# Kernel optimization log

Hardware: AMD Instinct MI355X
Metric: run time of the kernel (lower is better)

Reference implementation:

```python
import jax, jax.numpy as jnp
import numpy as np

B, TQ, TK, D, DV = 16, 2048, 2048, 128, 128
MASK_VAL = -1000000.0

def setup_inputs() -> dict:
    key = jax.random.key(0)
    kq, kk, kv, kl = jax.random.split(key, 4)
    q = jax.random.normal(kq, (B, TQ, D), dtype=jnp.float32)
    k = jax.random.normal(kk, (B, TK, D), dtype=jnp.float32)
    v = jax.random.normal(kv, (B, TK, DV), dtype=jnp.float32)
    valid_lens = jax.random.randint(kl, (B,), 1, TK, dtype=jnp.int64)
    return {"q": q, "k": k, "v": v, "valid_lens": valid_lens}

def reference(q, k, v, valid_lens):
    d = q.shape[-1]
    # scores: [B, Tq, Tk]
    scores = jnp.einsum('bqd,bkd->bqk', q, k) / jnp.sqrt(jnp.asarray(d, q.dtype))
    # mask key positions >= valid_len (same per-batch length for every query row)
    mask = jnp.arange(scores.shape[-1])[None, None, :] < valid_lens[:, None, None]
    scores = jnp.where(mask, scores, jnp.asarray(MASK_VAL, scores.dtype))
    attn = jax.nn.softmax(scores, axis=-1)
    # dropout p=0.0 (eval mode) -> identity
    return jnp.einsum('bqk,bkv->bqv', attn, v)
```

## Files before the change

### kernel.cpp

```cpp
#include <hip/hip_runtime.h>
#include <math.h>

#define NB 16
#define TQ 2048
#define TK 2048
#define DD 128
#define DVV 128

constexpr int QTILE = 128;
constexpr int KTILE = 32;
#define PSTR 40

typedef __attribute__((ext_vector_type(8))) _Float16 half8;
typedef __attribute__((ext_vector_type(4))) _Float16 half4;
typedef __attribute__((ext_vector_type(4))) float f32x4;

__device__ inline float fast_exp2(float x) {
#if __has_builtin(__builtin_amdgcn_exp2f)
    return __builtin_amdgcn_exp2f(x);
#else
    return exp2f(x);
#endif
}
__device__ inline void setprio1() { __builtin_amdgcn_s_setprio(1); }
__device__ inline void setprio0() { __builtin_amdgcn_s_setprio(0); }

__device__ inline void glds16(const _Float16* g, _Float16* l) {
    __builtin_amdgcn_global_load_lds(
        (const __attribute__((address_space(1))) void*)g,
        (__attribute__((address_space(3))) void*)l, 16, 0, 0);
}

__global__ __launch_bounds__(256)
void repack(const float* __restrict__ kg, const float* __restrict__ vg,
            const int* __restrict__ vlg,
            _Float16* __restrict__ Kpk, _Float16* __restrict__ Vpk)
{
    const int bt = blockIdx.x;
    const int b = bt >> 6, t = bt & 63;
    if (t * KTILE >= vlg[b]) return;
    const int tid = threadIdx.x;

    __shared__ float Vlds[32][129];

    const float* kin = kg + ((size_t)b * TK + t * KTILE) * DD;
    _Float16* kout = Kpk + ((size_t)bt << 12);
#pragma unroll
    for (int pp = 0; pp < 2; ++pp) {
        int s = tid + pp * 256;
        int ct = s >> 8, c = (s >> 6) & 3, ln = s & 63;
        int kr = ct * 16 + (ln & 15), kc = c * 32 + ((ln >> 4) & 3) * 8;
        const float* ip = kin + kr * DD + kc;
        float4 f0 = *(const float4*)ip;
        float4 f1 = *(const float4*)(ip + 4);
        half8 h;
        h[0] = (_Float16)f0.x; h[1] = (_Float16)f0.y;
        h[2] = (_Float16)f0.z; h[3] = (_Float16)f0.w;
        h[4] = (_Float16)f1.x; h[5] = (_Float16)f1.y;
        h[6] = (_Float16)f1.z; h[7] = (_Float16)f1.w;
        *(half8*)(kout + (size_t)s * 8) = h;
    }

    const float* vin = vg + ((size_t)b * TK + t * KTILE) * DVV;
#pragma unroll
    for (int pp = 0; pp < 4; ++pp) {
        int idx = tid + pp * 256;
        int r = idx >> 5, c4 = (idx & 31) * 4;
        float4 f = *(const float4*)(vin + r * DVV + c4);
        Vlds[r][c4 + 0] = f.x; Vlds[r][c4 + 1] = f.y;
        Vlds[r][c4 + 2] = f.z; Vlds[r][c4 + 3] = f.w;
    }
    __syncthreads();
    _Float16* vout = Vpk + ((size_t)bt << 12);
#pragma unroll
    for (int pp = 0; pp < 2; ++pp) {
        int s = tid + pp * 256;
        int n = s >> 6, ln = s & 63;
        int dv = n * 16 + (ln & 15), k0 = ((ln >> 4) & 3) * 8;
        half8 h;
#pragma unroll
        for (int j = 0; j < 8; ++j)
            h[j] = (_Float16)Vlds[k0 + j][dv];
        *(half8*)(vout + (size_t)s * 8) = h;
    }
}

__global__ __launch_bounds__(512, 6)
void attn_fwd(const float* __restrict__ qg,
              const _Float16* __restrict__ Kpk, const _Float16* __restrict__ Vpk,
              const int* __restrict__ vlg,
              float* __restrict__ outg, _Float16* __restrict__ wso,
              float* __restrict__ wsml, int ns)
{
    __shared__ _Float16 Kb[2][4096];
    __shared__ _Float16 Vb[2][4096];
    __shared__ _Float16 Plds[8][16][PSTR];

    const int tid  = threadIdx.x;
    const int wid  = tid >> 6;
    const int lane = tid & 63;
    const int l15  = lane & 15;
    const int lhi  = lane >> 4;

    const int bid   = blockIdx.x;
    const int b     = bid & (NB - 1);
    const int qbase = (bid >> 4) * QTILE;
    const int sp    = blockIdx.y;

    const int VL  = vlg[b];
    const int nkt = (VL + KTILE - 1) / KTILE;
    const int tps = (nkt + ns - 1) / ns;
    const int t0  = sp * tps;
    const int t1  = min(nkt, t0 + tps);
    if (t0 >= t1) return;

    const _Float16* ktb = Kpk + ((size_t)(b * 64) << 12);
    const _Float16* vtb = Vpk + ((size_t)(b * 64) << 12);

    half8 qf[4];
    {
        const float scale = 0.08838834764831845f * 1.4426950408889634f;
        const int qrow = qbase + wid * 16 + l15;
        const float* qp = qg + (size_t)(b * TQ + qrow) * DD + lhi * 8;
#pragma unroll
        for (int c = 0; c < 4; ++c) {
            float4 f0 = *(const float4*)(qp + c * 32);
            float4 f1 = *(const float4*)(qp + c * 32 + 4);
            half8 t;
            t[0] = (_Float16)(f0.x * scale); t[1] = (_Float16)(f0.y * scale);
            t[2] = (_Float16)(f0.z * scale); t[3] = (_Float16)(f0.w * scale);
            t[4] = (_Float16)(f1.x * scale); t[5] = (_Float16)(f1.y * scale);
            t[6] = (_Float16)(f1.z * scale); t[7] = (_Float16)(f1.w * scale);
            qf[c] = t;
        }
    }

    const int qtr = wid & 3;
    auto STAGE = [&](int buf, int t) {
        const _Float16* src = ((wid < 4) ? ktb : vtb)
                              + ((size_t)t << 12) + qtr * 1024 + lane * 8;
        _Float16* dst = (wid < 4) ? &Kb[buf][qtr * 1024] : &Vb[buf][qtr * 1024];
        glds16(src, dst);
        glds16(src + 512, dst + 512);
    };

    float m_i = -INFINITY, l_i = 0.f;
    f32x4 o[8];
#pragma unroll
    for (int n = 0; n < 8; ++n) { f32x4 z = {0.f, 0.f, 0.f, 0.f}; o[n] = z; }

    STAGE(0, t0);
    int cur = 0;
    for (int t = t0; t < t1; ++t) {
        const int kb = t * KTILE;
        const bool pre = (t + 1 < t1);
        if (pre) STAGE(cur ^ 1, t + 1);

        if (pre) asm volatile("s_waitcnt vmcnt(2)\ns_barrier" ::: "memory");
        else     asm volatile("s_waitcnt vmcnt(0)\ns_barrier" ::: "memory");

        const half8* kp = (const half8*)&Kb[cur][0];
        const half8* vp = (const half8*)&Vb[cur][0];

        f32x4 sc[2];
        setprio1();
#pragma unroll
        for (int ct = 0; ct < 2; ++ct) {
            f32x4 z = {0.f, 0.f, 0.f, 0.f};
            sc[ct] = z;
#pragma unroll
            for (int c = 0; c < 4; ++c) {
                half8 kf = kp[ct * 256 + c * 64 + lane];
                sc[ct] = __builtin_amdgcn_mfma_f32_16x16x32_f16(kf, qf[c], sc[ct], 0, 0, 0);
            }
        }
        setprio0();

        if (kb + KTILE > VL) {
#pragma unroll
            for (int ct = 0; ct < 2; ++ct) {
                const int kg = kb + ct * 16 + lhi * 4;
#pragma unroll
                for (int r = 0; r < 4; ++r)
                    if (kg + r >= VL) sc[ct][r] = -1e30f;
            }
        }

        float mx = sc[0][0];
#pragma unroll
        for (int ct = 0; ct < 2; ++ct)
#pragma unroll
            for (int r = 0; r < 4; ++r) mx = fmaxf(mx, sc[ct][r]);
        mx = fmaxf(mx, __shfl_xor(mx, 16));
        mx = fmaxf(mx, __shfl_xor(mx, 32));

        const bool skip = __all(mx <= m_i + 8.0f);
        const float mnew = skip ? m_i : fmaxf(m_i, mx);

        float p[8];
        float sum = 0.f;
#pragma unroll
        for (int ct = 0; ct < 2; ++ct)
#pragma unroll
            for (int r = 0; r < 4; ++r) {
                float e = fast_exp2(sc[ct][r] - mnew);
                p[ct * 4 + r] = e;
                sum += e;
            }
        sum += __shfl_xor(sum, 16);
        sum += __shfl_xor(sum, 32);

#pragma unroll
        for (int ct = 0; ct < 2; ++ct) {
            half4 ph;
            ph[0] = (_Float16)p[ct * 4 + 0]; ph[1] = (_Float16)p[ct * 4 + 1];
            ph[2] = (_Float16)p[ct * 4 + 2]; ph[3] = (_Float16)p[ct * 4 + 3];
            *(half4*)&Plds[wid][l15][ct * 16 + lhi * 4] = ph;
        }

        if (skip) {
            l_i += sum;
        } else {
            const float corr = fast_exp2(m_i - mnew);
            l_i = l_i * corr + sum;
            m_i = mnew;
            float cr[4];
#pragma unroll
            for (int r = 0; r < 4; ++r)
                cr[r] = __shfl(corr, (lane & 48) | (lhi * 4 + r));
#pragma unroll
            for (int n = 0; n < 8; ++n)
#pragma unroll
                for (int r = 0; r < 4; ++r) o[n][r] *= cr[r];
        }

        half8 pa = *(const half8*)&Plds[wid][l15][lhi * 8];
        setprio1();
#pragma unroll
        for (int n = 0; n < 8; ++n) {
            half8 vb = vp[n * 64 + lane];
            o[n] = __builtin_amdgcn_mfma_f32_16x16x32_f16(pa, vb, o[n], 0, 0, 0);
        }
        setprio0();

        asm volatile("s_waitcnt lgkmcnt(0)\ns_barrier" ::: "memory");
        cur ^= 1;
    }

    if (ns == 1) {
        float li4[4];
#pragma unroll
        for (int r = 0; r < 4; ++r) {
            float lr = __shfl(l_i, (lane & 48) | (lhi * 4 + r));
            li4[r] = 1.0f / lr;
        }
#pragma unroll
        for (int r = 0; r < 4; ++r) {
            const int qrow = qbase + wid * 16 + lhi * 4 + r;
            float* op = outg + (size_t)(b * TQ + qrow) * DVV + l15;
#pragma unroll
            for (int n = 0; n < 8; ++n)
                op[n * 16] = o[n][r] * li4[r];
        }
    } else {
        if (lhi == 0) {
            float2 ml = make_float2(m_i, l_i);
            *(float2*)&wsml[((size_t)(sp * NB + b) * TQ + qbase + wid * 16 + l15) * 2] = ml;
        }
        _Float16* po = wso + ((size_t)(sp * NB + b) * TQ + qbase + wid * 16) * DVV;
#pragma unroll
        for (int r = 0; r < 4; ++r)
#pragma unroll
            for (int n = 0; n < 8; ++n)
                po[(lhi * 4 + r) * DVV + n * 16 + l15] = (_Float16)o[n][r];
    }
}

__global__ __launch_bounds__(256)
void attn_combine(const _Float16* __restrict__ wso, const float* __restrict__ wsml,
                  const int* __restrict__ vlg, float* __restrict__ outg, int ns)
{
    const int idx = blockIdx.x * 256 + threadIdx.x;
    const int d8 = idx & 15;
    const int q  = (idx >> 4) & (TQ - 1);
    const int b  = idx >> 15;

    const int VL  = vlg[b];
    const int nkt = (VL + KTILE - 1) / KTILE;
    const int tps = (nkt + ns - 1) / ns;
    const int nv  = (nkt + tps - 1) / tps;

    float M = -1e30f, den = 0.f;
    float acc[8] = {0.f, 0.f, 0.f, 0.f, 0.f, 0.f, 0.f, 0.f};
    for (int s = 0; s < nv; ++s) {
        const size_t row = (size_t)(s * NB + b) * TQ + q;
        float2 ml = *(const float2*)&wsml[row * 2];
        float Mn = fmaxf(M, ml.x);
        float c  = fast_exp2(M - Mn);
        float w  = fast_exp2(ml.x - Mn);
        half8 ov = *(const half8*)&wso[row * DVV + d8 * 8];
#pragma unroll
        for (int j = 0; j < 8; ++j)
            acc[j] = acc[j] * c + (float)ov[j] * w;
        den = den * c + w * ml.y;
        M = Mn;
    }
    const float inv = 1.0f / den;
    float* op = outg + ((size_t)b * TQ + q) * DVV + d8 * 8;
    f32x4 r0 = {acc[0] * inv, acc[1] * inv, acc[2] * inv, acc[3] * inv};
    f32x4 r1 = {acc[4] * inv, acc[5] * inv, acc[6] * inv, acc[7] * inv};
    *(f32x4*)op = r0;
    *(f32x4*)(op + 4) = r1;
}

extern "C" void kernel_launch(void* const* d_in, const int* in_sizes, int n_in,
                              void* d_out, int out_size, void* d_ws, size_t ws_size,
                              hipStream_t stream) {
    const float* q  = (const float*)d_in[0];
    const float* k  = (const float*)d_in[1];
    const float* v  = (const float*)d_in[2];
    const int*   vl = (const int*)d_in[3];
    float* out = (float*)d_out;

    const size_t pk_elems = (size_t)NB * 64 * 4096;
    const size_t pk_bytes = 2 * pk_elems * sizeof(_Float16);
    const size_t o_elems  = (size_t)NB * TQ * DVV;
    const size_t ml_elems = (size_t)NB * TQ * 2;
    const size_t per_split = o_elems * sizeof(_Float16) + ml_elems * sizeof(float);

    int ns = 1;
    if (ws_size >= pk_bytes + 4 * per_split) ns = 4;
    else if (ws_size >= pk_bytes + 2 * per_split) ns = 2;

    _Float16* Kpk = (_Float16*)d_ws;
    _Float16* Vpk = Kpk + pk_elems;
    _Float16* wso  = Vpk + pk_elems;
    float*    wsml = (float*)(wso + (size_t)ns * o_elems);

    hipLaunchKernelGGL(repack, dim3(NB * 64), dim3(256), 0, stream,
                       k, v, vl, Kpk, Vpk);

    dim3 grid(NB * (TQ / QTILE), ns);
    hipLaunchKernelGGL(attn_fwd, grid, dim3(512), 0, stream,
                       q, Kpk, Vpk, vl, out, wso, wsml, ns);

    if (ns > 1) {
        dim3 cgrid((NB * TQ * 16) / 256);
        hipLaunchKernelGGL(attn_combine, cgrid, dim3(256), 0, stream,
                           wso, wsml, vl, out, ns);
    }
}
```

Before: 71.71 us.

## Switch attention to 32x32x16 MFMA with in-register P exchange and fixed-size KV splits

Moves QK^T and PV from 16x16x32 to 32x32x16 MFMA tiles, with each wave handling 32 query rows and the block shrunk to 4 waves. K and V are repacked to match. The P matrix is now converted to fp16 and exchanged between half-waves with cross-lane shuffles instead of a round trip through LDS, and the output is transposed through LDS so stores coalesce. KV splitting now uses a fixed tiles-per-split size (up to 8 splits) so short sequences launch fewer active blocks, at the cost of more accumulator registers per wave and lower occupancy.

Result: slower. 75.01 us (+4.6%).

```diff
diff --git a/kernel.cpp b/kernel.cpp
--- a/kernel.cpp
+++ b/kernel.cpp
@@ -7,23 +7,23 @@
 #define DD 128
 #define DVV 128
 
+constexpr int KTILE = 32;
 constexpr int QTILE = 128;
-constexpr int KTILE = 32;
-#define PSTR 40
 
 typedef __attribute__((ext_vector_type(8))) _Float16 half8;
-typedef __attribute__((ext_vector_type(4))) _Float16 half4;
+typedef __attribute__((ext_vector_type(16))) float f32x16;
 typedef __attribute__((ext_vector_type(4))) float f32x4;
 
-__device__ inline float fast_exp2(float x) {
-#if __has_builtin(__builtin_amdgcn_exp2f)
-    return __builtin_amdgcn_exp2f(x);
-#else
-    return exp2f(x);
-#endif
-}
+__device__ inline float fast_exp2(float x) { return __builtin_amdgcn_exp2f(x); }
 __device__ inline void setprio1() { __builtin_amdgcn_s_setprio(1); }
 __device__ inline void setprio0() { __builtin_amdgcn_s_setprio(0); }
+
+__device__ inline unsigned pk2(float a, float b) {
+    auto h = __builtin_amdgcn_cvt_pkrtz(a, b);
+    unsigned u;
+    __builtin_memcpy(&u, &h, 4);
+    return u;
+}
 
 __device__ inline void glds16(const _Float16* g, _Float16* l) {
     __builtin_amdgcn_global_load_lds(
@@ -48,17 +48,17 @@
 #pragma unroll
     for (int pp = 0; pp < 2; ++pp) {
         int s = tid + pp * 256;
-        int ct = s >> 8, c = (s >> 6) & 3, ln = s & 63;
-        int kr = ct * 16 + (ln & 15), kc = c * 32 + ((ln >> 4) & 3) * 8;
-        const float* ip = kin + kr * DD + kc;
+        int c = s >> 6, l = s & 63;
+        int row = l & 31, d0 = c * 16 + (l >> 5) * 8;
+        const float* ip = kin + row * DD + d0;
         float4 f0 = *(const float4*)ip;
         float4 f1 = *(const float4*)(ip + 4);
-        half8 h;
-        h[0] = (_Float16)f0.x; h[1] = (_Float16)f0.y;
-        h[2] = (_Float16)f0.z; h[3] = (_Float16)f0.w;
-        h[4] = (_Float16)f1.x; h[5] = (_Float16)f1.y;
-        h[6] = (_Float16)f1.z; h[7] = (_Float16)f1.w;
-        *(half8*)(kout + (size_t)s * 8) = h;
+        half8 hh;
+        hh[0] = (_Float16)f0.x; hh[1] = (_Float16)f0.y;
+        hh[2] = (_Float16)f0.z; hh[3] = (_Float16)f0.w;
+        hh[4] = (_Float16)f1.x; hh[5] = (_Float16)f1.y;
+        hh[6] = (_Float16)f1.z; hh[7] = (_Float16)f1.w;
+        *(half8*)(kout + (size_t)s * 8) = hh;
     }
 
     const float* vin = vg + ((size_t)b * TK + t * KTILE) * DVV;
@@ -75,79 +75,79 @@
 #pragma unroll
     for (int pp = 0; pp < 2; ++pp) {
         int s = tid + pp * 256;
-        int n = s >> 6, ln = s & 63;
-        int dv = n * 16 + (ln & 15), k0 = ((ln >> 4) & 3) * 8;
-        half8 h;
+        int sv = s >> 6, l = s & 63;
+        int dv = (sv >> 1) * 32 + (l & 31);
+        int k0 = (sv & 1) * 16 + (l >> 5) * 8;
+        half8 hh;
 #pragma unroll
         for (int j = 0; j < 8; ++j)
-            h[j] = (_Float16)Vlds[k0 + j][dv];
-        *(half8*)(vout + (size_t)s * 8) = h;
-    }
-}
-
-__global__ __launch_bounds__(512, 6)
+            hh[j] = (_Float16)Vlds[k0 + j][dv];
+        *(half8*)(vout + (size_t)s * 8) = hh;
+    }
+}
+
+__global__ __launch_bounds__(256, 3)
 void attn_fwd(const float* __restrict__ qg,
               const _Float16* __restrict__ Kpk, const _Float16* __restrict__ Vpk,
               const int* __restrict__ vlg,
               float* __restrict__ outg, _Float16* __restrict__ wso,
-              float* __restrict__ wsml, int ns)
+              float* __restrict__ wsml, int nsplit, int tpb)
 {
-    __shared__ _Float16 Kb[2][4096];
-    __shared__ _Float16 Vb[2][4096];
-    __shared__ _Float16 Plds[8][16][PSTR];
+    __shared__ __align__(16) _Float16 smem[16384];
 
     const int tid  = threadIdx.x;
     const int wid  = tid >> 6;
     const int lane = tid & 63;
-    const int l15  = lane & 15;
-    const int lhi  = lane >> 4;
-
-    const int bid   = blockIdx.x;
-    const int b     = bid & (NB - 1);
-    const int qbase = (bid >> 4) * QTILE;
+    const int l31  = lane & 31;
+    const int hi   = lane >> 5;
+
+    const int b     = blockIdx.x & (NB - 1);
+    const int qbase = (blockIdx.x >> 4) * QTILE;
     const int sp    = blockIdx.y;
 
     const int VL  = vlg[b];
     const int nkt = (VL + KTILE - 1) / KTILE;
-    const int tps = (nkt + ns - 1) / ns;
-    const int t0  = sp * tps;
-    const int t1  = min(nkt, t0 + tps);
+    const int t0  = sp * tpb;
+    const int t1  = min(nkt, t0 + tpb);
     if (t0 >= t1) return;
 
     const _Float16* ktb = Kpk + ((size_t)(b * 64) << 12);
     const _Float16* vtb = Vpk + ((size_t)(b * 64) << 12);
 
-    half8 qf[4];
+    half8 qf[8];
     {
         const float scale = 0.08838834764831845f * 1.4426950408889634f;
-        const int qrow = qbase + wid * 16 + l15;
-        const float* qp = qg + (size_t)(b * TQ + qrow) * DD + lhi * 8;
-#pragma unroll
-        for (int c = 0; c < 4; ++c) {
-            float4 f0 = *(const float4*)(qp + c * 32);
-            float4 f1 = *(const float4*)(qp + c * 32 + 4);
-            half8 t;
-            t[0] = (_Float16)(f0.x * scale); t[1] = (_Float16)(f0.y * scale);
-            t[2] = (_Float16)(f0.z * scale); t[3] = (_Float16)(f0.w * scale);
-            t[4] = (_Float16)(f1.x * scale); t[5] = (_Float16)(f1.y * scale);
-            t[6] = (_Float16)(f1.z * scale); t[7] = (_Float16)(f1.w * scale);
-            qf[c] = t;
-        }
-    }
-
-    const int qtr = wid & 3;
+        const float* qp = qg + (size_t)(b * TQ + qbase + wid * 32 + l31) * DD;
+#pragma unroll
+        for (int c = 0; c < 8; ++c) {
+            int d0 = c * 16 + hi * 8;
+            float4 f0 = *(const float4*)(qp + d0);
+            float4 f1 = *(const float4*)(qp + d0 + 4);
+            half8 tq;
+            tq[0] = (_Float16)(f0.x * scale); tq[1] = (_Float16)(f0.y * scale);
+            tq[2] = (_Float16)(f0.z * scale); tq[3] = (_Float16)(f0.w * scale);
+            tq[4] = (_Float16)(f1.x * scale); tq[5] = (_Float16)(f1.y * scale);
+            tq[6] = (_Float16)(f1.z * scale); tq[7] = (_Float16)(f1.w * scale);
+            qf[c] = tq;
+        }
+    }
+
     auto STAGE = [&](int buf, int t) {
-        const _Float16* src = ((wid < 4) ? ktb : vtb)
-                              + ((size_t)t << 12) + qtr * 1024 + lane * 8;
-        _Float16* dst = (wid < 4) ? &Kb[buf][qtr * 1024] : &Vb[buf][qtr * 1024];
-        glds16(src, dst);
-        glds16(src + 512, dst + 512);
+        const bool isK = wid < 2;
+        const int hf = wid & 1;
+        const _Float16* src = (isK ? ktb : vtb) + ((size_t)t << 12) + hf * 2048 + lane * 8;
+        _Float16* dst = smem + (isK ? 0 : 8192) + buf * 4096 + hf * 2048;
+#pragma unroll
+        for (int u = 0; u < 4; ++u)
+            glds16(src + u * 512, dst + u * 512);
     };
 
     float m_i = -INFINITY, l_i = 0.f;
-    f32x4 o[8];
-#pragma unroll
-    for (int n = 0; n < 8; ++n) { f32x4 z = {0.f, 0.f, 0.f, 0.f}; o[n] = z; }
+    f32x16 o[4];
+#pragma unroll
+    for (int n = 0; n < 4; ++n)
+#pragma unroll
+        for (int r = 0; r < 16; ++r) o[n][r] = 0.f;
 
     STAGE(0, t0);
     int cur = 0;
@@ -156,67 +156,61 @@
         const bool pre = (t + 1 < t1);
         if (pre) STAGE(cur ^ 1, t + 1);
 
-        if (pre) asm volatile("s_waitcnt vmcnt(2)\ns_barrier" ::: "memory");
+        if (pre) asm volatile("s_waitcnt vmcnt(4)\ns_barrier" ::: "memory");
         else     asm volatile("s_waitcnt vmcnt(0)\ns_barrier" ::: "memory");
 
-        const half8* kp = (const half8*)&Kb[cur][0];
-        const half8* vp = (const half8*)&Vb[cur][0];
-
-        f32x4 sc[2];
+        const _Float16* kbuf = smem + cur * 4096;
+        const _Float16* vbuf = smem + 8192 + cur * 4096;
+
+        f32x16 sc;
+#pragma unroll
+        for (int r = 0; r < 16; ++r) sc[r] = 0.f;
         setprio1();
 #pragma unroll
-        for (int ct = 0; ct < 2; ++ct) {
-            f32x4 z = {0.f, 0.f, 0.f, 0.f};
-            sc[ct] = z;
-#pragma unroll
-            for (int c = 0; c < 4; ++c) {
-                half8 kf = kp[ct * 256 + c * 64 + lane];
-                sc[ct] = __builtin_amdgcn_mfma_f32_16x16x32_f16(kf, qf[c], sc[ct], 0, 0, 0);
+        for (int c = 0; c < 8; ++c) {
+            half8 kf = *(const half8*)(kbuf + c * 512 + lane * 8);
+            sc = __builtin_amdgcn_mfma_f32_32x32x16_f16(kf, qf[c], sc, 0, 0, 0);
+        }
+        setprio0();
+
+        if (kb + KTILE > VL) {
+#pragma unroll
+            for (int r = 0; r < 16; ++r) {
+                int rowk = kb + (r & 3) + 8 * (r >> 2) + 4 * hi;
+                if (rowk >= VL) sc[r] = -1e30f;
             }
         }
-        setprio0();
-
-        if (kb + KTILE > VL) {
-#pragma unroll
-            for (int ct = 0; ct < 2; ++ct) {
-                const int kg = kb + ct * 16 + lhi * 4;
-#pragma unroll
-                for (int r = 0; r < 4; ++r)
-                    if (kg + r >= VL) sc[ct][r] = -1e30f;
-            }
-        }
-
-        float mx = sc[0][0];
-#pragma unroll
-        for (int ct = 0; ct < 2; ++ct)
-#pragma unroll
-            for (int r = 0; r < 4; ++r) mx = fmaxf(mx, sc[ct][r]);
-        mx = fmaxf(mx, __shfl_xor(mx, 16));
+
+        float mx = sc[0];
+#pragma unroll
+        for (int r = 1; r < 16; ++r) mx = fmaxf(mx, sc[r]);
         mx = fmaxf(mx, __shfl_xor(mx, 32));
 
         const bool skip = __all(mx <= m_i + 8.0f);
         const float mnew = skip ? m_i : fmaxf(m_i, mx);
 
-        float p[8];
+        float p[16];
         float sum = 0.f;
 #pragma unroll
-        for (int ct = 0; ct < 2; ++ct)
-#pragma unroll
-            for (int r = 0; r < 4; ++r) {
-                float e = fast_exp2(sc[ct][r] - mnew);
-                p[ct * 4 + r] = e;
-                sum += e;
-            }
-        sum += __shfl_xor(sum, 16);
+        for (int r = 0; r < 16; ++r) {
+            p[r] = fast_exp2(sc[r] - mnew);
+            sum += p[r];
+        }
         sum += __shfl_xor(sum, 32);
 
-#pragma unroll
-        for (int ct = 0; ct < 2; ++ct) {
-            half4 ph;
-            ph[0] = (_Float16)p[ct * 4 + 0]; ph[1] = (_Float16)p[ct * 4 + 1];
-            ph[2] = (_Float16)p[ct * 4 + 2]; ph[3] = (_Float16)p[ct * 4 + 3];
-            *(half4*)&Plds[wid][l15][ct * 16 + lhi * 4] = ph;
-        }
+        unsigned a0 = pk2(p[0],  p[1]),  a1 = pk2(p[2],  p[3]);
+        unsigned a2 = pk2(p[4],  p[5]),  a3 = pk2(p[6],  p[7]);
+        unsigned b0 = pk2(p[8],  p[9]),  b1 = pk2(p[10], p[11]);
+        unsigned b2 = pk2(p[12], p[13]), b3 = pk2(p[14], p[15]);
+        unsigned pa0 = __shfl_xor(a0, 32), pa1 = __shfl_xor(a1, 32);
+        unsigned pa2 = __shfl_xor(a2, 32), pa3 = __shfl_xor(a3, 32);
+        unsigned pb0 = __shfl_xor(b0, 32), pb1 = __shfl_xor(b1, 32);
+        unsigned pb2 = __shfl_xor(b2, 32), pb3 = __shfl_xor(b3, 32);
+        union PF { unsigned u[4]; half8 v; } pf0, pf1;
+        pf0.u[0] = hi ? pa2 : a0;  pf0.u[1] = hi ? pa3 : a1;
+        pf0.u[2] = hi ? a2  : pa0; pf0.u[3] = hi ? a3  : pa1;
+        pf1.u[0] = hi ? pb2 : b0;  pf1.u[1] = hi ? pb3 : b1;
+        pf1.u[2] = hi ? b2  : pb0; pf1.u[3] = hi ? b3  : pb1;
 
         if (skip) {
             l_i += sum;
@@ -224,22 +218,19 @@
             const float corr = fast_exp2(m_i - mnew);
             l_i = l_i * corr + sum;
             m_i = mnew;
-            float cr[4];
-#pragma unroll
-            for (int r = 0; r < 4; ++r)
-                cr[r] = __shfl(corr, (lane & 48) | (lhi * 4 + r));
-#pragma unroll
-            for (int n = 0; n < 8; ++n)
-#pragma unroll
-                for (int r = 0; r < 4; ++r) o[n][r] *= cr[r];
-        }
-
-        half8 pa = *(const half8*)&Plds[wid][l15][lhi * 8];
+#pragma unroll
+            for (int n = 0; n < 4; ++n)
+#pragma unroll
+                for (int r = 0; r < 16; ++r) o[n][r] *= corr;
+        }
+
         setprio1();
 #pragma unroll
-        for (int n = 0; n < 8; ++n) {
-            half8 vb = vp[n * 64 + lane];
-            o[n] = __builtin_amdgcn_mfma_f32_16x16x32_f16(pa, vb, o[n], 0, 0, 0);
+        for (int n = 0; n < 4; ++n) {
+            half8 v0 = *(const half8*)(vbuf + (n * 2 + 0) * 512 + lane * 8);
+            o[n] = __builtin_amdgcn_mfma_f32_32x32x16_f16(v0, pf0.v, o[n], 0, 0, 0);
+            half8 v1 = *(const half8*)(vbuf + (n * 2 + 1) * 512 + lane * 8);
+            o[n] = __builtin_amdgcn_mfma_f32_32x32x16_f16(v1, pf1.v, o[n], 0, 0, 0);
         }
         setprio0();
 
@@ -247,38 +238,43 @@
         cur ^= 1;
     }
 
-    if (ns == 1) {
-        float li4[4];
-#pragma unroll
-        for (int r = 0; r < 4; ++r) {
-            float lr = __shfl(l_i, (lane & 48) | (lhi * 4 + r));
-            li4[r] = 1.0f / lr;
-        }
-#pragma unroll
-        for (int r = 0; r < 4; ++r) {
-            const int qrow = qbase + wid * 16 + lhi * 4 + r;
-            float* op = outg + (size_t)(b * TQ + qrow) * DVV + l15;
-#pragma unroll
-            for (int n = 0; n < 8; ++n)
-                op[n * 16] = o[n][r] * li4[r];
-        }
-    } else {
-        if (lhi == 0) {
-            float2 ml = make_float2(m_i, l_i);
-            *(float2*)&wsml[((size_t)(sp * NB + b) * TQ + qbase + wid * 16 + l15) * 2] = ml;
-        }
-        _Float16* po = wso + ((size_t)(sp * NB + b) * TQ + qbase + wid * 16) * DVV;
-#pragma unroll
-        for (int r = 0; r < 4; ++r)
-#pragma unroll
-            for (int n = 0; n < 8; ++n)
-                po[(lhi * 4 + r) * DVV + n * 16 + l15] = (_Float16)o[n][r];
+    const float inv = (nsplit == 1) ? (1.0f / l_i) : 1.0f;
+    float* tp = (float*)smem + wid * 1056;
+#pragma unroll
+    for (int n = 0; n < 4; ++n) {
+#pragma unroll
+        for (int r = 0; r < 16; ++r) {
+            int row = (r & 3) + 8 * (r >> 2) + 4 * hi;
+            tp[l31 * 33 + row] = o[n][r] * inv;
+        }
+        asm volatile("s_waitcnt lgkmcnt(0)" ::: "memory");
+        if (nsplit == 1) {
+            float* op = outg + (size_t)(b * TQ + qbase + wid * 32) * DVV + n * 32 + l31;
+#pragma unroll
+            for (int rr = 0; rr < 16; ++rr) {
+                int qq = rr * 2 + hi;
+                op[(size_t)qq * DVV] = tp[qq * 33 + l31];
+            }
+        } else {
+            _Float16* po = wso + ((size_t)(sp * NB + b) * TQ + qbase + wid * 32) * DVV
+                           + n * 32 + l31;
+#pragma unroll
+            for (int rr = 0; rr < 16; ++rr) {
+                int qq = rr * 2 + hi;
+                po[(size_t)qq * DVV] = (_Float16)tp[qq * 33 + l31];
+            }
+        }
+        asm volatile("s_waitcnt lgkmcnt(0)" ::: "memory");
+    }
+    if (nsplit > 1 && hi == 0) {
+        int q = qbase + wid * 32 + l31;
+        *(float2*)&wsml[((size_t)(sp * NB + b) * TQ + q) * 2] = make_float2(m_i, l_i);
     }
 }
 
 __global__ __launch_bounds__(256)
 void attn_combine(const _Float16* __restrict__ wso, const float* __restrict__ wsml,
-                  const int* __restrict__ vlg, float* __restrict__ outg, int ns)
+                  const int* __restrict__ vlg, float* __restrict__ outg, int tpb)
 {
     const int idx = blockIdx.x * 256 + threadIdx.x;
     const int d8 = idx & 15;
@@ -287,8 +283,7 @@
 
     const int VL  = vlg[b];
     const int nkt = (VL + KTILE - 1) / KTILE;
-    const int tps = (nkt + ns - 1) / ns;
-    const int nv  = (nkt + tps - 1) / tps;
+    const int nv  = (nkt + tpb - 1) / tpb;
 
     float M = -1e30f, den = 0.f;
     float acc[8] = {0.f, 0.f, 0.f, 0.f, 0.f, 0.f, 0.f, 0.f};
@@ -322,31 +317,33 @@
     const int*   vl = (const int*)d_in[3];
     float* out = (float*)d_out;
 
-    const size_t pk_elems = (size_t)NB * 64 * 4096;
-    const size_t pk_bytes = 2 * pk_elems * sizeof(_Float16);
-    const size_t o_elems  = (size_t)NB * TQ * DVV;
-    const size_t ml_elems = (size_t)NB * TQ * 2;
-    const size_t per_split = o_elems * sizeof(_Float16) + ml_elems * sizeof(float);
+    const size_t pk_elems  = (size_t)NB * 64 * 4096;
+    const size_t pk_bytes  = 2 * pk_elems * sizeof(_Float16);
+    const size_t o_elems   = (size_t)NB * TQ * DVV;
+    const size_t per_split = o_elems * sizeof(_Float16)
+                           + (size_t)NB * TQ * 2 * sizeof(float);
 
     int ns = 1;
-    if (ws_size >= pk_bytes + 4 * per_split) ns = 4;
+    if      (ws_size >= pk_bytes + 8 * per_split) ns = 8;
+    else if (ws_size >= pk_bytes + 4 * per_split) ns = 4;
     else if (ws_size >= pk_bytes + 2 * per_split) ns = 2;
+    const int tpb = 64 / ns;
 
     _Float16* Kpk = (_Float16*)d_ws;
     _Float16* Vpk = Kpk + pk_elems;
-    _Float16* wso  = Vpk + pk_elems;
-    float*    wsml = (float*)(wso + (size_t)ns * o_elems);
+    _Float16* wso = Vpk + pk_elems;
+    float*   wsml = (float*)(wso + (size_t)ns * o_elems);
 
     hipLaunchKernelGGL(repack, dim3(NB * 64), dim3(256), 0, stream,
                        k, v, vl, Kpk, Vpk);
 
     dim3 grid(NB * (TQ / QTILE), ns);
-    hipLaunchKernelGGL(attn_fwd, grid, dim3(512), 0, stream,
-                       q, Kpk, Vpk, vl, out, wso, wsml, ns);
+    hipLaunchKernelGGL(attn_fwd, grid, dim3(256), 0, stream,
+                       q, Kpk, Vpk, vl, out, wso, wsml, ns, tpb);
 
     if (ns > 1) {
         dim3 cgrid((NB * TQ * 16) / 256);
         hipLaunchKernelGGL(attn_combine, cgrid, dim3(256), 0, stream,
-                           wso, wsml, vl, out, ns);
-    }
-}
+                           wso, wsml, vl, out, tpb);
+    }
+}
```
